# Performance work log

Hardware: AMD Instinct MI355X
Metric: run time of the kernel (lower is better)

The kernel has to match this reference:

```python
import jax, jax.numpy as jnp
import numpy as np


def setup_inputs() -> dict:
    key = jax.random.key(0)
    k1_key, k2_key = jax.random.split(key)
    C_OUT, C_IN, NB, K = 64, 64, 4, 15
    k1 = jax.random.normal(k1_key, (C_OUT * NB, C_IN * NB, K, K), dtype=jnp.float32)
    k2 = jax.random.normal(k2_key, (C_OUT * NB, C_IN * NB, K, K), dtype=jnp.float32)
    return {"k1": k1, "k2": k2, "n_blades": NB}


def _blade_conv(x, w):
    # x: [nb, nb, K, K] treated as NCHW batch, w: [nb, nb, K, K] treated as OIHW filter
    return jax.lax.conv(x, w, window_strides=(1, 1), padding="SAME")


def reference(k1, k2, n_blades):
    A, B, K, _ = k1.shape
    co, ci = A // n_blades, B // n_blades
    # (co*nb, ci*nb, K, K) -> (co, ci, nb, nb, K, K)
    a = k1.reshape(co, n_blades, ci, n_blades, K, K).transpose(0, 2, 1, 3, 4, 5)
    b = k2.reshape(co, n_blades, ci, n_blades, K, K).transpose(0, 2, 1, 3, 4, 5)
    # double vmap over (co, ci): each is a tiny nb x nb SAME conv
    k = jax.vmap(jax.vmap(_blade_conv))(a, b)  # (co, ci, nb, nb, K, K)
    k = k.transpose(0, 2, 1, 3, 4, 5).reshape(co * n_blades, ci * n_blades, K, K)
    return k
```

## Files before the change

### kernel.cpp

```cpp
#include <hip/hip_runtime.h>


typedef float f32x4 __attribute__((ext_vector_type(4)));
typedef __bf16 bf16x8 __attribute__((ext_vector_type(8)));

#define KS 15
#define SP 225
#define NCH 256
#define RSTRIDE 56
#define ROWS 183
#define APAD_SHORTS (ROWS * RSTRIDE)
#define TBL_OFF (APAD_SHORTS * 2)
#define TBL_UPC 496
#define ARENA_B (TBL_OFF + 4 * TBL_UPC * 8)

__device__ __forceinline__ unsigned short f2bf(float f) {
    unsigned u = __builtin_bit_cast(unsigned, f);
    u += 0x7FFFu + ((u >> 16) & 1u);
    return (unsigned short)(u >> 16);
}

__global__ __launch_bounds__(256, 4)
void blade_conv_mfma(const float* __restrict__ k1,
                     const float* __restrict__ k2,
                     float* __restrict__ out) {
    __shared__ __align__(16) unsigned char arena[ARENA_B];
    unsigned short*     Apad  = (unsigned short*)arena;
    unsigned long long* tbl   = (unsigned long long*)(arena + TBL_OFF);
    float*              slabs = (float*)arena;

    const int tid  = threadIdx.x;
    const int lane = tid & 63;
    const int wid  = tid >> 6;
    const int co = blockIdx.x, ci = blockIdx.y;

    f32x4 z = {0.f, 0.f, 0.f, 0.f};
    for (int i = tid; i < ARENA_B / 16; i += 256) ((f32x4*)arena)[i] = z;
    __syncthreads();

    for (int idx = tid; idx < 16 * SP; idx += 256) {
        int nc = idx / SP, rem = idx % SP;
        int y = rem / KS, x = rem % KS;
        int n = nc >> 2, c = nc & 3;
        float v = k1[((size_t)((co * 4 + n) * NCH + ci * 4 + c)) * SP + rem];
        int band = n * 2 + (c >> 1), side = c & 1;
        Apad[(band * 22 + 7 + y) * RSTRIDE + side * 24 + 7 + x] = f2bf(v);
    }

    for (int idx = tid; idx < 4 * SP; idx += 256) {
        int c = idx / SP, rem = idx % SP;
        int ky = rem / KS, kx = rem % KS;
        size_t base = ((size_t)(co * 4) * NCH + ci * 4 + c) * SP + rem;
        float v0 = k2[base];
        float v1 = k2[base + (size_t)NCH * SP];
        float v2 = k2[base + 2 * (size_t)NCH * SP];
        float v3 = k2[base + 3 * (size_t)NCH * SP];
        unsigned lo = (unsigned)f2bf(v0) | ((unsigned)f2bf(v1) << 16);
        unsigned hi = (unsigned)f2bf(v2) | ((unsigned)f2bf(v3) << 16);
        tbl[c * TBL_UPC + 32 * ky + kx + 15] =
            (unsigned long long)lo | ((unsigned long long)hi << 32);
    }
    __syncthreads();

    f32x4 acc[4][4];
    #pragma unroll
    for (int n = 0; n < 4; ++n)
        #pragma unroll
        for (int o = 0; o < 4; ++o)
            acc[n][o] = z;

    const int yl    = lane & 15;
    const int kg    = lane >> 4;
    const int side_w = wid & 1, whalf = wid >> 1;
    const int acol  = side_w * 24 + (kg << 3);
    const unsigned long long* tbase =
        &tbl[wid * TBL_UPC + (kg << 3) - yl + 15];

    #pragma unroll
    for (int ky = 0; ky < 15; ++ky) {
        bf16x8 af[4];
        #pragma unroll
        for (int n = 0; n < 4; ++n) {
            int band = n * 2 + whalf;
            af[n] = *(const bf16x8*)&Apad[(band * 22 + yl + ky) * RSTRIDE + acol];
        }
        unsigned long long q[8];
        #pragma unroll
        for (int j = 0; j < 8; ++j) q[j] = tbase[32 * ky + j];

        union { bf16x8 v; unsigned u[4]; } bo0, bo1, bo2, bo3;
        #pragma unroll
        for (int t = 0; t < 4; ++t) {
            unsigned a0 = (unsigned)q[2 * t],         a1 = (unsigned)q[2 * t + 1];
            unsigned b0 = (unsigned)(q[2 * t] >> 32), b1 = (unsigned)(q[2 * t + 1] >> 32);
            bo0.u[t] = __builtin_amdgcn_perm(a1, a0, 0x05040100u);
            bo1.u[t] = __builtin_amdgcn_perm(a1, a0, 0x07060302u);
            bo2.u[t] = __builtin_amdgcn_perm(b1, b0, 0x05040100u);
            bo3.u[t] = __builtin_amdgcn_perm(b1, b0, 0x07060302u);
        }
        #pragma unroll
        for (int n = 0; n < 4; ++n) {
            acc[n][0] = __builtin_amdgcn_mfma_f32_16x16x32_bf16(af[n], bo0.v, acc[n][0], 0, 0, 0);
            acc[n][1] = __builtin_amdgcn_mfma_f32_16x16x32_bf16(af[n], bo1.v, acc[n][1], 0, 0, 0);
            acc[n][2] = __builtin_amdgcn_mfma_f32_16x16x32_bf16(af[n], bo2.v, acc[n][2], 0, 0, 0);
            acc[n][3] = __builtin_amdgcn_mfma_f32_16x16x32_bf16(af[n], bo3.v, acc[n][3], 0, 0, 0);
        }
    }

    const int xl = lane & 15;
    #pragma unroll
    for (int g = 0; g < 4; ++g) {
        __syncthreads();
        {
            float* slab = slabs + wid * 1280;
            #pragma unroll
            for (int o = 0; o < 4; ++o)
                *(f32x4*)&slab[(o * 16 + xl) * 20 + (kg << 2)] = acc[g][o];
        }
        __syncthreads();
        for (int idx = tid; idx < 4 * SP; idx += 256) {
            int o = idx / SP, rem = idx % SP;
            int yy = rem / KS, xx = rem % KS;
            int soff = (o * 16 + xx) * 20 + yy;
            float s = slabs[soff] + slabs[1280 + soff]
                    + slabs[2560 + soff] + slabs[3840 + soff];
            out[((size_t)((co * 4 + g) * NCH + ci * 4 + o)) * SP + rem] = s;
        }
    }
}

extern "C" void kernel_launch(void* const* d_in, const int* in_sizes, int n_in,
                              void* d_out, int out_size, void* d_ws, size_t ws_size,
                              hipStream_t stream) {
    (void)in_sizes; (void)n_in; (void)d_ws; (void)ws_size; (void)out_size;
    const float* k1 = (const float*)d_in[0];
    const float* k2 = (const float*)d_in[1];
    float* out = (float*)d_out;

    dim3 grid(64, 64, 1);
    dim3 block(256, 1, 1);
    hipLaunchKernelGGL(blade_conv_mfma, grid, block, 0, stream, k1, k2, out);
}
```

Before: 77.52 us.

## Split each block over output-blade halves to double grid and cut LDS

```diff
diff --git a/kernel.cpp b/kernel.cpp
--- a/kernel.cpp
+++ b/kernel.cpp
@@ -8,7 +8,7 @@
 #define SP 225
 #define NCH 256
 #define RSTRIDE 56
-#define ROWS 183
+#define ROWS 95
 #define APAD_SHORTS (ROWS * RSTRIDE)
 #define TBL_OFF (APAD_SHORTS * 2)
 #define TBL_UPC 496
@@ -20,7 +20,7 @@
     return (unsigned short)(u >> 16);
 }
 
-__global__ __launch_bounds__(256, 4)
+__global__ __launch_bounds__(256, 5)
 void blade_conv_mfma(const float* __restrict__ k1,
                      const float* __restrict__ k2,
                      float* __restrict__ out) {
@@ -32,18 +32,20 @@
     const int tid  = threadIdx.x;
     const int lane = tid & 63;
     const int wid  = tid >> 6;
-    const int co = blockIdx.x, ci = blockIdx.y;
+    const int zh = blockIdx.x & 1;
+    const int co = blockIdx.x >> 1, ci = blockIdx.y;
 
     f32x4 z = {0.f, 0.f, 0.f, 0.f};
     for (int i = tid; i < ARENA_B / 16; i += 256) ((f32x4*)arena)[i] = z;
     __syncthreads();
 
-    for (int idx = tid; idx < 16 * SP; idx += 256) {
+    for (int idx = tid; idx < 8 * SP; idx += 256) {
         int nc = idx / SP, rem = idx % SP;
         int y = rem / KS, x = rem % KS;
-        int n = nc >> 2, c = nc & 3;
+        int np = nc >> 2, c = nc & 3;
+        int n = zh * 2 + np;
         float v = k1[((size_t)((co * 4 + n) * NCH + ci * 4 + c)) * SP + rem];
-        int band = n * 2 + (c >> 1), side = c & 1;
+        int band = np * 2 + (c >> 1), side = c & 1;
         Apad[(band * 22 + 7 + y) * RSTRIDE + side * 24 + 7 + x] = f2bf(v);
     }
 
@@ -62,12 +64,12 @@
     }
     __syncthreads();
 
-    f32x4 acc[4][4];
+    f32x4 acc[2][4];
     #pragma unroll
-    for (int n = 0; n < 4; ++n)
+    for (int np = 0; np < 2; ++np)
         #pragma unroll
         for (int o = 0; o < 4; ++o)
-            acc[n][o] = z;
+            acc[np][o] = z;
 
     const int yl    = lane & 15;
     const int kg    = lane >> 4;
@@ -78,11 +80,11 @@
 
     #pragma unroll
     for (int ky = 0; ky < 15; ++ky) {
-        bf16x8 af[4];
+        bf16x8 af[2];
         #pragma unroll
-        for (int n = 0; n < 4; ++n) {
-            int band = n * 2 + whalf;
-            af[n] = *(const bf16x8*)&Apad[(band * 22 + yl + ky) * RSTRIDE + acol];
+        for (int np = 0; np < 2; ++np) {
+            int band = np * 2 + whalf;
+            af[np] = *(const bf16x8*)&Apad[(band * 22 + yl + ky) * RSTRIDE + acol];
         }
         unsigned long long q[8];
         #pragma unroll
@@ -99,17 +101,17 @@
             bo3.u[t] = __builtin_amdgcn_perm(b1, b0, 0x07060302u);
         }
         #pragma unroll
-        for (int n = 0; n < 4; ++n) {
-            acc[n][0] = __builtin_amdgcn_mfma_f32_16x16x32_bf16(af[n], bo0.v, acc[n][0], 0, 0, 0);
-            acc[n][1] = __builtin_amdgcn_mfma_f32_16x16x32_bf16(af[n], bo1.v, acc[n][1], 0, 0, 0);
-            acc[n][2] = __builtin_amdgcn_mfma_f32_16x16x32_bf16(af[n], bo2.v, acc[n][2], 0, 0, 0);
-            acc[n][3] = __builtin_amdgcn_mfma_f32_16x16x32_bf16(af[n], bo3.v, acc[n][3], 0, 0, 0);
+        for (int np = 0; np < 2; ++np) {
+            acc[np][0] = __builtin_amdgcn_mfma_f32_16x16x32_bf16(af[np], bo0.v, acc[np][0], 0, 0, 0);
+            acc[np][1] = __builtin_amdgcn_mfma_f32_16x16x32_bf16(af[np], bo1.v, acc[np][1], 0, 0, 0);
+            acc[np][2] = __builtin_amdgcn_mfma_f32_16x16x32_bf16(af[np], bo2.v, acc[np][2], 0, 0, 0);
+            acc[np][3] = __builtin_amdgcn_mfma_f32_16x16x32_bf16(af[np], bo3.v, acc[np][3], 0, 0, 0);
         }
     }
 
     const int xl = lane & 15;
     #pragma unroll
-    for (int g = 0; g < 4; ++g) {
+    for (int g = 0; g < 2; ++g) {
         __syncthreads();
         {
             float* slab = slabs + wid * 1280;
@@ -124,7 +126,8 @@
             int soff = (o * 16 + xx) * 20 + yy;
             float s = slabs[soff] + slabs[1280 + soff]
                     + slabs[2560 + soff] + slabs[3840 + soff];
-            out[((size_t)((co * 4 + g) * NCH + ci * 4 + o)) * SP + rem] = s;
+            int n = zh * 2 + g;
+            out[((size_t)((co * 4 + n) * NCH + ci * 4 + o)) * SP + rem] = s;
         }
     }
 }
@@ -137,7 +140,7 @@
     const float* k2 = (const float*)d_in[1];
     float* out = (float*)d_out;
 
-    dim3 grid(64, 64, 1);
+    dim3 grid(128, 64, 1);
     dim3 block(256, 1, 1);
     hipLaunchKernelGGL(blade_conv_mfma, grid, block, 0, stream, k1, k2, out);
 }
```

Result: slower. 84.29 us (+8.7%).

## Double block to 512 threads, splitting output blades across two wave groups

Applied to the files above, without the earlier changes.

```diff
diff --git a/kernel.cpp b/kernel.cpp
--- a/kernel.cpp
+++ b/kernel.cpp
@@ -20,7 +20,7 @@
     return (unsigned short)(u >> 16);
 }
 
-__global__ __launch_bounds__(256, 4)
+__global__ __launch_bounds__(512, 6)
 void blade_conv_mfma(const float* __restrict__ k1,
                      const float* __restrict__ k2,
                      float* __restrict__ out) {
@@ -32,57 +32,63 @@
     const int tid  = threadIdx.x;
     const int lane = tid & 63;
     const int wid  = tid >> 6;
+    const int c_w  = wid & 3;
+    const int np   = wid >> 2;
     const int co = blockIdx.x, ci = blockIdx.y;
 
     f32x4 z = {0.f, 0.f, 0.f, 0.f};
-    for (int i = tid; i < ARENA_B / 16; i += 256) ((f32x4*)arena)[i] = z;
+    for (int i = tid; i < ARENA_B / 16; i += 512) ((f32x4*)arena)[i] = z;
     __syncthreads();
 
-    for (int idx = tid; idx < 16 * SP; idx += 256) {
-        int nc = idx / SP, rem = idx % SP;
-        int y = rem / KS, x = rem % KS;
-        int n = nc >> 2, c = nc & 3;
-        float v = k1[((size_t)((co * 4 + n) * NCH + ci * 4 + c)) * SP + rem];
-        int band = n * 2 + (c >> 1), side = c & 1;
-        Apad[(band * 22 + 7 + y) * RSTRIDE + side * 24 + 7 + x] = f2bf(v);
-    }
-
-    for (int idx = tid; idx < 4 * SP; idx += 256) {
-        int c = idx / SP, rem = idx % SP;
-        int ky = rem / KS, kx = rem % KS;
-        size_t base = ((size_t)(co * 4) * NCH + ci * 4 + c) * SP + rem;
-        float v0 = k2[base];
-        float v1 = k2[base + (size_t)NCH * SP];
-        float v2 = k2[base + 2 * (size_t)NCH * SP];
-        float v3 = k2[base + 3 * (size_t)NCH * SP];
-        unsigned lo = (unsigned)f2bf(v0) | ((unsigned)f2bf(v1) << 16);
-        unsigned hi = (unsigned)f2bf(v2) | ((unsigned)f2bf(v3) << 16);
-        tbl[c * TBL_UPC + 32 * ky + kx + 15] =
-            (unsigned long long)lo | ((unsigned long long)hi << 32);
+    {
+        const int lo = tid & 255, half = tid >> 8;
+        if (lo < 225) {
+            const int y = lo / 15, x = lo - y * 15;
+            #pragma unroll
+            for (int j = 0; j < 8; ++j) {
+                int n = 2 * half + (j >> 2), cc = j & 3;
+                float v = k1[((size_t)((co * 4 + n) * NCH + ci * 4 + cc)) * SP + lo];
+                int band = n * 2 + (cc >> 1), side = cc & 1;
+                Apad[(band * 22 + 7 + y) * RSTRIDE + side * 24 + 7 + x] = f2bf(v);
+            }
+            #pragma unroll
+            for (int jj = 0; jj < 2; ++jj) {
+                int cc = 2 * half + jj;
+                size_t base = ((size_t)(co * 4) * NCH + ci * 4 + cc) * SP + lo;
+                float v0 = k2[base];
+                float v1 = k2[base + (size_t)NCH * SP];
+                float v2 = k2[base + 2 * (size_t)NCH * SP];
+                float v3 = k2[base + 3 * (size_t)NCH * SP];
+                unsigned lw = (unsigned)f2bf(v0) | ((unsigned)f2bf(v1) << 16);
+                unsigned hw = (unsigned)f2bf(v2) | ((unsigned)f2bf(v3) << 16);
+                tbl[cc * TBL_UPC + 32 * y + x + 15] =
+                    (unsigned long long)lw | ((unsigned long long)hw << 32);
+            }
+        }
     }
     __syncthreads();
 
-    f32x4 acc[4][4];
+    f32x4 acc[2][4];
     #pragma unroll
-    for (int n = 0; n < 4; ++n)
+    for (int g = 0; g < 2; ++g)
         #pragma unroll
         for (int o = 0; o < 4; ++o)
-            acc[n][o] = z;
+            acc[g][o] = z;
 
     const int yl    = lane & 15;
     const int kg    = lane >> 4;
-    const int side_w = wid & 1, whalf = wid >> 1;
+    const int side_w = c_w & 1, whalf = c_w >> 1;
     const int acol  = side_w * 24 + (kg << 3);
     const unsigned long long* tbase =
-        &tbl[wid * TBL_UPC + (kg << 3) - yl + 15];
+        &tbl[c_w * TBL_UPC + (kg << 3) - yl + 15];
 
     #pragma unroll
     for (int ky = 0; ky < 15; ++ky) {
-        bf16x8 af[4];
+        bf16x8 af[2];
         #pragma unroll
-        for (int n = 0; n < 4; ++n) {
-            int band = n * 2 + whalf;
-            af[n] = *(const bf16x8*)&Apad[(band * 22 + yl + ky) * RSTRIDE + acol];
+        for (int g = 0; g < 2; ++g) {
+            int band = (2 * np + g) * 2 + whalf;
+            af[g] = *(const bf16x8*)&Apad[(band * 22 + yl + ky) * RSTRIDE + acol];
         }
         unsigned long long q[8];
         #pragma unroll
@@ -99,32 +105,36 @@
             bo3.u[t] = __builtin_amdgcn_perm(b1, b0, 0x07060302u);
         }
         #pragma unroll
-        for (int n = 0; n < 4; ++n) {
-            acc[n][0] = __builtin_amdgcn_mfma_f32_16x16x32_bf16(af[n], bo0.v, acc[n][0], 0, 0, 0);
-            acc[n][1] = __builtin_amdgcn_mfma_f32_16x16x32_bf16(af[n], bo1.v, acc[n][1], 0, 0, 0);
-            acc[n][2] = __builtin_amdgcn_mfma_f32_16x16x32_bf16(af[n], bo2.v, acc[n][2], 0, 0, 0);
-            acc[n][3] = __builtin_amdgcn_mfma_f32_16x16x32_bf16(af[n], bo3.v, acc[n][3], 0, 0, 0);
+        for (int g = 0; g < 2; ++g) {
+            acc[g][0] = __builtin_amdgcn_mfma_f32_16x16x32_bf16(af[g], bo0.v, acc[g][0], 0, 0, 0);
+            acc[g][1] = __builtin_amdgcn_mfma_f32_16x16x32_bf16(af[g], bo1.v, acc[g][1], 0, 0, 0);
+            acc[g][2] = __builtin_amdgcn_mfma_f32_16x16x32_bf16(af[g], bo2.v, acc[g][2], 0, 0, 0);
+            acc[g][3] = __builtin_amdgcn_mfma_f32_16x16x32_bf16(af[g], bo3.v, acc[g][3], 0, 0, 0);
         }
     }
 
     const int xl = lane & 15;
     #pragma unroll
-    for (int g = 0; g < 4; ++g) {
+    for (int r = 0; r < 4; ++r) {
+        const int g = r >> 1, op = r & 1;
         __syncthreads();
         {
-            float* slab = slabs + wid * 1280;
+            float* slab = slabs + wid * 640;
             #pragma unroll
-            for (int o = 0; o < 4; ++o)
-                *(f32x4*)&slab[(o * 16 + xl) * 20 + (kg << 2)] = acc[g][o];
+            for (int oi = 0; oi < 2; ++oi)
+                *(f32x4*)&slab[(oi * 16 + xl) * 20 + (kg << 2)] = acc[g][2 * op + oi];
         }
         __syncthreads();
-        for (int idx = tid; idx < 4 * SP; idx += 256) {
-            int o = idx / SP, rem = idx % SP;
-            int yy = rem / KS, xx = rem % KS;
-            int soff = (o * 16 + xx) * 20 + yy;
-            float s = slabs[soff] + slabs[1280 + soff]
-                    + slabs[2560 + soff] + slabs[3840 + soff];
-            out[((size_t)((co * 4 + g) * NCH + ci * 4 + o)) * SP + rem] = s;
+        for (int idx = tid; idx < 900; idx += 512) {
+            int q4 = idx / 225;
+            int rem = idx - q4 * 225;
+            int np_g = q4 >> 1, oi = q4 & 1;
+            int yy = rem / 15, xx = rem - yy * 15;
+            int soff = (oi * 16 + xx) * 20 + yy;
+            const float* sb = slabs + np_g * 2560;
+            float s = sb[soff] + sb[640 + soff] + sb[1280 + soff] + sb[1920 + soff];
+            int n = 2 * np_g + g, o = 2 * op + oi;
+            out[((size_t)((co * 4 + n) * NCH + ci * 4 + o)) * SP + rem] = s;
         }
     }
 }
@@ -138,6 +148,6 @@
     float* out = (float*)d_out;
 
     dim3 grid(64, 64, 1);
-    dim3 block(256, 1, 1);
+    dim3 block(512, 1, 1);
     hipLaunchKernelGGL(blade_conv_mfma, grid, block, 0, stream, k1, k2, out);
 }
```

New measurement: 77.58 us. About the same (+0.1%).
